# Kernel optimization log

Hardware: AMD Instinct MI355X
Metric: run time of the kernel (lower is better)

## Reference

```python
import jax, jax.numpy as jnp
import numpy as np

MARGIN = 0.1
N = 16384


def setup_inputs() -> dict:
    key = jax.random.key(0)
    k1, k2 = jax.random.split(key)
    pred = jax.random.normal(k1, (N,), dtype=jnp.float32)
    target = jax.random.uniform(k2, (N,), dtype=jnp.float32)
    return {"pred": pred, "target": target}


def reference(pred, target):
    # mask[i, j] = target[j] < target[i]  (the Python loop's Tj per row i)
    mask = target[None, :] < target[:, None]            # [N, N] bool
    # hinge[i, j] = max(0, margin - (pred[i] - pred[j]))
    hinge = jnp.maximum(0.0, MARGIN - (pred[:, None] - pred[None, :]))
    row_sum = jnp.sum(jnp.where(mask, hinge, 0.0), axis=1)   # [N]
    cnt = jnp.sum(mask, axis=1)                               # [N] int
    # rows with no j such that target[j] < target[i] are skipped (continue)
    per_row = jnp.where(cnt > 0, row_sum / jnp.maximum(cnt, 1).astype(pred.dtype), 0.0)
    return jnp.sum(per_row) / pred.shape[0]
```

## Files before the change

### kernel.cpp

```cpp
#include <hip/hip_runtime.h>


constexpr float MARGIN = 0.1f;
constexpr int NBINS  = 4096;
constexpr int RT     = 16;
constexpr int T      = 256;
constexpr int NSLOTS = 256;

__device__ __forceinline__ int bin_of(float t) {
    int b = (int)(t * (float)NBINS);
    b = b < 0 ? 0 : b;
    b = b > NBINS - 1 ? NBINS - 1 : b;
    return b;
}

__global__ __launch_bounds__(256) void zero_ws(int* __restrict__ hist,
                                               float* __restrict__ partials) {
    int i = blockIdx.x * 256 + (int)threadIdx.x;
    if (i < NBINS) hist[i] = 0;
    int j = i - NBINS;
    if (j >= 0 && j < NSLOTS) partials[j] = 0.f;
}

__global__ __launch_bounds__(256) void hist_k(const float* __restrict__ target,
                                              int* __restrict__ hist, int n) {
    int i = blockIdx.x * 256 + (int)threadIdx.x;
    if (i < n) atomicAdd(&hist[bin_of(target[i])], 1);
}

__global__ __launch_bounds__(1024) void scan_k(const int* __restrict__ hist,
                                               int* __restrict__ B,
                                               int* __restrict__ cur) {
    __shared__ int part[1024];
    const int t = (int)threadIdx.x;
    int h0 = hist[4 * t + 0], h1 = hist[4 * t + 1];
    int h2 = hist[4 * t + 2], h3 = hist[4 * t + 3];
    int tot = h0 + h1 + h2 + h3;
    part[t] = tot;
    __syncthreads();
    for (int off = 1; off < 1024; off <<= 1) {
        int v = (t >= off) ? part[t - off] : 0;
        __syncthreads();
        part[t] += v;
        __syncthreads();
    }
    int excl = part[t] - tot;
    int b0 = excl, b1 = b0 + h0, b2 = b1 + h1, b3 = b2 + h2;
    B[4 * t + 0] = b0; B[4 * t + 1] = b1; B[4 * t + 2] = b2; B[4 * t + 3] = b3;
    cur[4 * t + 0] = b0; cur[4 * t + 1] = b1; cur[4 * t + 2] = b2; cur[4 * t + 3] = b3;
    if (t == 1023) B[4096] = part[1023];
}

__global__ __launch_bounds__(256) void scatter_k(const float* __restrict__ pred,
                                                 const float* __restrict__ target,
                                                 float* __restrict__ ts,
                                                 float* __restrict__ ps,
                                                 int* __restrict__ cur, int n) {
    int i = blockIdx.x * 256 + (int)threadIdx.x;
    if (i < n) {
        float t = target[i], p = pred[i];
        int pos = atomicAdd(&cur[bin_of(t)], 1);
        ts[pos] = t;
        ps[pos] = p;
    }
}

__global__ __launch_bounds__(T) void rank_sorted(const float* __restrict__ ts,
                                                 const float* __restrict__ ps,
                                                 const int* __restrict__ B,
                                                 float* __restrict__ partials, int n) {
    const int g = (int)gridDim.x - 1 - (int)blockIdx.x;
    const int q = g * RT;

    float ti[RT], ci[RT];
    #pragma unroll
    for (int r = 0; r < RT; ++r) {
        ti[r] = ts[q + r];
        ci[r] = MARGIN - ps[q + r];
    }

    const int Blo = B[bin_of(ti[0])];
    const int Bhi = B[bin_of(ti[RT - 1]) + 1];
    const int M0 = Blo & ~3;
    int M1 = (Bhi + 3) & ~3;
    if (M1 > n) M1 = n;

    float sum[RT];
    #pragma unroll
    for (int r = 0; r < RT; ++r) sum[r] = 0.f;

    const float4* __restrict__ p4 = (const float4*)ps;
    const float4* __restrict__ t4 = (const float4*)ts;

    const int f4 = M0 >> 2;
    for (int j = (int)threadIdx.x; j < f4; j += T) {
        const float4 pj = p4[j];
        #pragma unroll
        for (int r = 0; r < RT; ++r) {
            sum[r] += fmaxf(0.f, ci[r] + pj.x);
            sum[r] += fmaxf(0.f, ci[r] + pj.y);
            sum[r] += fmaxf(0.f, ci[r] + pj.z);
            sum[r] += fmaxf(0.f, ci[r] + pj.w);
        }
    }

    unsigned int cnt[RT];
    #pragma unroll
    for (int r = 0; r < RT; ++r) cnt[r] = 0u;

    const int m4lo = M0 >> 2, m4hi = M1 >> 2;
    const int iters = (m4hi - m4lo + T - 1) / T;
    for (int it = 0; it < iters; ++it) {
        const int j = m4lo + it * T + (int)threadIdx.x;
        const bool inb = j < m4hi;
        const int jc = inb ? j : m4lo;
        const float4 tj = t4[jc];
        const float4 pj = p4[jc];
        #pragma unroll
        for (int r = 0; r < RT; ++r) {
            { bool m = inb && (tj.x < ti[r]); float h = fmaxf(0.f, ci[r] + pj.x);
              sum[r] += m ? h : 0.f; cnt[r] += (unsigned)__popcll(__ballot(m)); }
            { bool m = inb && (tj.y < ti[r]); float h = fmaxf(0.f, ci[r] + pj.y);
              sum[r] += m ? h : 0.f; cnt[r] += (unsigned)__popcll(__ballot(m)); }
            { bool m = inb && (tj.z < ti[r]); float h = fmaxf(0.f, ci[r] + pj.z);
              sum[r] += m ? h : 0.f; cnt[r] += (unsigned)__popcll(__ballot(m)); }
            { bool m = inb && (tj.w < ti[r]); float h = fmaxf(0.f, ci[r] + pj.w);
              sum[r] += m ? h : 0.f; cnt[r] += (unsigned)__popcll(__ballot(m)); }
        }
    }

    __shared__ float ls[T / 64][RT];
    __shared__ unsigned int lc[T / 64][RT];
    const int lane = (int)threadIdx.x & 63;
    const int wv   = (int)threadIdx.x >> 6;
    #pragma unroll
    for (int r = 0; r < RT; ++r) {
        float s = sum[r];
        #pragma unroll
        for (int off = 32; off > 0; off >>= 1) s += __shfl_down(s, off, 64);
        if (lane == 0) { ls[wv][r] = s; lc[wv][r] = cnt[r]; }
    }
    __syncthreads();

    __shared__ float vrow[RT];
    if ((int)threadIdx.x < RT) {
        float s = 0.f;
        unsigned int c = (unsigned int)M0;
        #pragma unroll
        for (int w = 0; w < T / 64; ++w) { s += ls[w][threadIdx.x]; c += lc[w][threadIdx.x]; }
        vrow[threadIdx.x] = (c > 0u) ? s / (float)c : 0.f;
    }
    __syncthreads();
    if (threadIdx.x == 0) {
        float v = 0.f;
        #pragma unroll
        for (int r = 0; r < RT; ++r) v += vrow[r];
        atomicAdd(&partials[blockIdx.x & (NSLOTS - 1)], v);
    }
}

__global__ __launch_bounds__(NSLOTS) void final_k(const float* __restrict__ partials,
                                                  float* __restrict__ out, int n) {
    float s = partials[threadIdx.x];
    #pragma unroll
    for (int off = 32; off > 0; off >>= 1) s += __shfl_down(s, off, 64);
    __shared__ float sd[NSLOTS / 64];
    const int lane = (int)threadIdx.x & 63, wv = (int)threadIdx.x >> 6;
    if (lane == 0) sd[wv] = s;
    __syncthreads();
    if (threadIdx.x == 0) {
        float t = 0.f;
        #pragma unroll
        for (int w = 0; w < NSLOTS / 64; ++w) t += sd[w];
        out[0] = t / (float)n;
    }
}

extern "C" void kernel_launch(void* const* d_in, const int* in_sizes, int n_in,
                              void* d_out, int out_size, void* d_ws, size_t ws_size,
                              hipStream_t stream) {
    const float* pred   = (const float*)d_in[0];
    const float* target = (const float*)d_in[1];
    const int n = in_sizes[0];

    char* w = (char*)d_ws;
    size_t o = 0;
    float* ts       = (float*)(w + o); o += (size_t)n * 4;
    float* ps       = (float*)(w + o); o += (size_t)n * 4;
    int*   hist     = (int*)(w + o);   o += (size_t)NBINS * 4;
    int*   B        = (int*)(w + o);   o += (size_t)(NBINS + 4) * 4;
    int*   cur      = (int*)(w + o);   o += (size_t)NBINS * 4;
    float* partials = (float*)(w + o);

    zero_ws<<<(NBINS + NSLOTS + 255) / 256, 256, 0, stream>>>(hist, partials);
    hist_k<<<(n + 255) / 256, 256, 0, stream>>>(target, hist, n);
    scan_k<<<1, 1024, 0, stream>>>(hist, B, cur);
    scatter_k<<<(n + 255) / 256, 256, 0, stream>>>(pred, target, ts, ps, cur, n);
    rank_sorted<<<n / RT, T, 0, stream>>>(ts, ps, B, partials, n);
    final_k<<<1, NSLOTS, 0, stream>>>(partials, (float*)d_out, n);
}
```

Before: 88.71 us.

## Fuse histogram scan into scatter and fold final reduction into rank kernel

Cuts the six-launch pipeline to three kernels. Per-block shared-memory histograms with a column-major count table let each scatter block compute its own bin bases and block offsets, which replaces the separate zero, scan and global-atomic scatter passes. The final sum moves into the rank kernel through a done counter, with the last block to finish doing the reduction in double. In exchange, every scatter block rereads the full per-block count table, and only 32 blocks work on the histogram and scatter stages.

```diff
diff --git a/kernel.cpp b/kernel.cpp
--- a/kernel.cpp
+++ b/kernel.cpp
@@ -2,74 +2,112 @@
 
 
 constexpr float MARGIN = 0.1f;
-constexpr int NBINS  = 4096;
-constexpr int RT     = 16;
-constexpr int T      = 256;
-constexpr int NSLOTS = 256;
+constexpr int NBINS = 4096;
+constexpr int HB    = 32;
+constexpr int RT    = 16;
+constexpr int T     = 256;
 
 __device__ __forceinline__ int bin_of(float t) {
     int b = (int)(t * (float)NBINS);
-    b = b < 0 ? 0 : b;
-    b = b > NBINS - 1 ? NBINS - 1 : b;
+    b = b < 0 ? 0 : (b > NBINS - 1 ? NBINS - 1 : b);
     return b;
 }
 
-__global__ __launch_bounds__(256) void zero_ws(int* __restrict__ hist,
-                                               float* __restrict__ partials) {
-    int i = blockIdx.x * 256 + (int)threadIdx.x;
-    if (i < NBINS) hist[i] = 0;
-    int j = i - NBINS;
-    if (j >= 0 && j < NSLOTS) partials[j] = 0.f;
-}
-
-__global__ __launch_bounds__(256) void hist_k(const float* __restrict__ target,
-                                              int* __restrict__ hist, int n) {
-    int i = blockIdx.x * 256 + (int)threadIdx.x;
-    if (i < n) atomicAdd(&hist[bin_of(target[i])], 1);
-}
-
-__global__ __launch_bounds__(1024) void scan_k(const int* __restrict__ hist,
-                                               int* __restrict__ B,
-                                               int* __restrict__ cur) {
-    __shared__ int part[1024];
-    const int t = (int)threadIdx.x;
-    int h0 = hist[4 * t + 0], h1 = hist[4 * t + 1];
-    int h2 = hist[4 * t + 2], h3 = hist[4 * t + 3];
-    int tot = h0 + h1 + h2 + h3;
-    part[t] = tot;
-    __syncthreads();
-    for (int off = 1; off < 1024; off <<= 1) {
-        int v = (t >= off) ? part[t - off] : 0;
-        __syncthreads();
-        part[t] += v;
-        __syncthreads();
-    }
-    int excl = part[t] - tot;
-    int b0 = excl, b1 = b0 + h0, b2 = b1 + h1, b3 = b2 + h2;
-    B[4 * t + 0] = b0; B[4 * t + 1] = b1; B[4 * t + 2] = b2; B[4 * t + 3] = b3;
-    cur[4 * t + 0] = b0; cur[4 * t + 1] = b1; cur[4 * t + 2] = b2; cur[4 * t + 3] = b3;
-    if (t == 1023) B[4096] = part[1023];
-}
-
-__global__ __launch_bounds__(256) void scatter_k(const float* __restrict__ pred,
-                                                 const float* __restrict__ target,
-                                                 float* __restrict__ ts,
-                                                 float* __restrict__ ps,
-                                                 int* __restrict__ cur, int n) {
-    int i = blockIdx.x * 256 + (int)threadIdx.x;
-    if (i < n) {
-        float t = target[i], p = pred[i];
-        int pos = atomicAdd(&cur[bin_of(t)], 1);
+__global__ __launch_bounds__(T) void hist_k(const float* __restrict__ target,
+                                            int* __restrict__ H, int n) {
+    __shared__ int lh[NBINS];
+    for (int i = (int)threadIdx.x; i < NBINS; i += T) lh[i] = 0;
+    __syncthreads();
+    const int per  = n / HB;
+    const int base = (int)blockIdx.x * per;
+    for (int i = (int)threadIdx.x; i < per; i += T)
+        atomicAdd(&lh[bin_of(target[base + i])], 1);
+    __syncthreads();
+    for (int i = (int)threadIdx.x; i < NBINS; i += T)
+        H[i * HB + (int)blockIdx.x] = lh[i];
+}
+
+__global__ __launch_bounds__(T) void scatter_k(const float* __restrict__ pred,
+                                               const float* __restrict__ target,
+                                               const int* __restrict__ H,
+                                               float* __restrict__ ts,
+                                               float* __restrict__ ps,
+                                               int* __restrict__ Bg,
+                                               int* __restrict__ done, int n) {
+    __shared__ int bbase[NBINS];
+    __shared__ int prevk[NBINS];
+    __shared__ int lcnt[NBINS];
+    __shared__ int wsum[T / 64];
+
+    const int tid = (int)threadIdx.x;
+    const int k   = (int)blockIdx.x;
+    constexpr int BPT = NBINS / T;
+    const int b0 = tid * BPT;
+
+    int tot[BPT], prv[BPT];
+    int s = 0;
+    #pragma unroll
+    for (int u = 0; u < BPT; ++u) {
+        const int b = b0 + u;
+        const int4* h4 = (const int4*)(H + b * HB);
+        int t = 0, pv = 0;
+        #pragma unroll
+        for (int q = 0; q < HB / 4; ++q) {
+            int4 v = h4[q];
+            t += v.x + v.y + v.z + v.w;
+            const int blk = q * 4;
+            pv += (blk + 0 < k ? v.x : 0) + (blk + 1 < k ? v.y : 0)
+                + (blk + 2 < k ? v.z : 0) + (blk + 3 < k ? v.w : 0);
+        }
+        tot[u] = t; prv[u] = pv; s += t;
+        lcnt[b] = 0;
+    }
+
+    int incl = s;
+    #pragma unroll
+    for (int off = 1; off < 64; off <<= 1) {
+        int v = __shfl_up(incl, off, 64);
+        if ((tid & 63) >= off) incl += v;
+    }
+    if ((tid & 63) == 63) wsum[tid >> 6] = incl;
+    __syncthreads();
+    int woff = 0;
+    for (int w = 0; w < (tid >> 6); ++w) woff += wsum[w];
+    int run = woff + incl - s;
+    #pragma unroll
+    for (int u = 0; u < BPT; ++u) {
+        bbase[b0 + u] = run;
+        prevk[b0 + u] = prv[u];
+        run += tot[u];
+    }
+    __syncthreads();
+
+    const int per  = n / HB;
+    const int base = k * per;
+    for (int i = tid; i < per; i += T) {
+        const float t = target[base + i];
+        const float p = pred[base + i];
+        const int b = bin_of(t);
+        const int r = atomicAdd(&lcnt[b], 1);
+        const int pos = bbase[b] + prevk[b] + r;
         ts[pos] = t;
         ps[pos] = p;
     }
-}
-
-__global__ __launch_bounds__(T) void rank_sorted(const float* __restrict__ ts,
-                                                 const float* __restrict__ ps,
-                                                 const int* __restrict__ B,
-                                                 float* __restrict__ partials, int n) {
-    const int g = (int)gridDim.x - 1 - (int)blockIdx.x;
+
+    if (k == 0) {
+        for (int b = tid; b < NBINS; b += T) Bg[b] = bbase[b];
+        if (tid == 0) { Bg[NBINS] = n; done[0] = 0; }
+    }
+}
+
+__global__ __launch_bounds__(T) void rank_k(const float* __restrict__ ts,
+                                            const float* __restrict__ ps,
+                                            const int* __restrict__ B,
+                                            float* __restrict__ partials,
+                                            int* __restrict__ done,
+                                            float* __restrict__ out, int n) {
+    const int nblk = (int)gridDim.x;
+    const int g = nblk - 1 - (int)blockIdx.x;
     const int q = g * RT;
 
     float ti[RT], ci[RT];
@@ -135,44 +173,50 @@
     const int wv   = (int)threadIdx.x >> 6;
     #pragma unroll
     for (int r = 0; r < RT; ++r) {
-        float s = sum[r];
-        #pragma unroll
-        for (int off = 32; off > 0; off >>= 1) s += __shfl_down(s, off, 64);
-        if (lane == 0) { ls[wv][r] = s; lc[wv][r] = cnt[r]; }
-    }
-    __syncthreads();
-
-    __shared__ float vrow[RT];
+        float sv = sum[r];
+        #pragma unroll
+        for (int off = 32; off > 0; off >>= 1) sv += __shfl_down(sv, off, 64);
+        if (lane == 0) { ls[wv][r] = sv; lc[wv][r] = cnt[r]; }
+    }
+    __syncthreads();
+
+    float val = 0.f;
     if ((int)threadIdx.x < RT) {
-        float s = 0.f;
+        float sv = 0.f;
         unsigned int c = (unsigned int)M0;
         #pragma unroll
-        for (int w = 0; w < T / 64; ++w) { s += ls[w][threadIdx.x]; c += lc[w][threadIdx.x]; }
-        vrow[threadIdx.x] = (c > 0u) ? s / (float)c : 0.f;
-    }
-    __syncthreads();
+        for (int w = 0; w < T / 64; ++w) { sv += ls[w][threadIdx.x]; c += lc[w][threadIdx.x]; }
+        val = (c > 0u) ? sv / (float)c : 0.f;
+    }
+    if ((int)threadIdx.x < 64) {
+        #pragma unroll
+        for (int off = 8; off > 0; off >>= 1) val += __shfl_down(val, off, 64);
+    }
+    if (threadIdx.x == 0) partials[blockIdx.x] = val;
+
+    __threadfence();
+    __shared__ int lastflag;
     if (threadIdx.x == 0) {
-        float v = 0.f;
-        #pragma unroll
-        for (int r = 0; r < RT; ++r) v += vrow[r];
-        atomicAdd(&partials[blockIdx.x & (NSLOTS - 1)], v);
-    }
-}
-
-__global__ __launch_bounds__(NSLOTS) void final_k(const float* __restrict__ partials,
-                                                  float* __restrict__ out, int n) {
-    float s = partials[threadIdx.x];
-    #pragma unroll
-    for (int off = 32; off > 0; off >>= 1) s += __shfl_down(s, off, 64);
-    __shared__ float sd[NSLOTS / 64];
-    const int lane = (int)threadIdx.x & 63, wv = (int)threadIdx.x >> 6;
-    if (lane == 0) sd[wv] = s;
-    __syncthreads();
-    if (threadIdx.x == 0) {
-        float t = 0.f;
-        #pragma unroll
-        for (int w = 0; w < NSLOTS / 64; ++w) t += sd[w];
-        out[0] = t / (float)n;
+        const int old = atomicAdd(done, 1);
+        lastflag = (old == nblk - 1) ? 1 : 0;
+    }
+    __syncthreads();
+    if (lastflag) {
+        __threadfence();
+        const volatile float* vp = partials;
+        double sd_acc = 0.0;
+        for (int i = (int)threadIdx.x; i < nblk; i += T) sd_acc += (double)vp[i];
+        #pragma unroll
+        for (int off = 32; off > 0; off >>= 1) sd_acc += __shfl_down(sd_acc, off, 64);
+        __shared__ double sd[T / 64];
+        if (lane == 0) sd[wv] = sd_acc;
+        __syncthreads();
+        if (threadIdx.x == 0) {
+            double tt = 0.0;
+            #pragma unroll
+            for (int w = 0; w < T / 64; ++w) tt += sd[w];
+            out[0] = (float)(tt / (double)n);
+        }
     }
 }
 
@@ -182,20 +226,23 @@
     const float* pred   = (const float*)d_in[0];
     const float* target = (const float*)d_in[1];
     const int n = in_sizes[0];
+    const int nblk = n / RT;
 
     char* w = (char*)d_ws;
     size_t o = 0;
-    float* ts       = (float*)(w + o); o += (size_t)n * 4;
-    float* ps       = (float*)(w + o); o += (size_t)n * 4;
-    int*   hist     = (int*)(w + o);   o += (size_t)NBINS * 4;
-    int*   B        = (int*)(w + o);   o += (size_t)(NBINS + 4) * 4;
-    int*   cur      = (int*)(w + o);   o += (size_t)NBINS * 4;
-    float* partials = (float*)(w + o);
-
-    zero_ws<<<(NBINS + NSLOTS + 255) / 256, 256, 0, stream>>>(hist, partials);
-    hist_k<<<(n + 255) / 256, 256, 0, stream>>>(target, hist, n);
-    scan_k<<<1, 1024, 0, stream>>>(hist, B, cur);
-    scatter_k<<<(n + 255) / 256, 256, 0, stream>>>(pred, target, ts, ps, cur, n);
-    rank_sorted<<<n / RT, T, 0, stream>>>(ts, ps, B, partials, n);
-    final_k<<<1, NSLOTS, 0, stream>>>(partials, (float*)d_out, n);
-}
+    auto alloc = [&](size_t bytes) {
+        void* p = w + o;
+        o = (o + bytes + 255) & ~(size_t)255;
+        return p;
+    };
+    float* ts       = (float*)alloc((size_t)n * 4);
+    float* ps       = (float*)alloc((size_t)n * 4);
+    int*   H        = (int*)alloc((size_t)NBINS * HB * 4);
+    int*   B        = (int*)alloc((size_t)(NBINS + 1) * 4);
+    float* partials = (float*)alloc((size_t)nblk * 4);
+    int*   done     = (int*)alloc(16);
+
+    hist_k<<<HB, T, 0, stream>>>(target, H, n);
+    scatter_k<<<HB, T, 0, stream>>>(pred, target, H, ts, ps, B, done, n);
+    rank_k<<<nblk, T, 0, stream>>>(ts, ps, B, partials, done, (float*)d_out, n);
+}
```

Result: slower. 181.6 us (+104.8%).
